# Kernel tuning notes

Hardware: AMD Instinct MI355X
Metric: run time of the kernel (lower is better)

The kernel has to match this reference:

```python
import jax, jax.numpy as jnp
import numpy as np

NUM_LEVELS = 8
CODEBOOK_SIZE = 1024
D_MODEL = 512


def setup_inputs() -> dict:
    key = jax.random.key(0)
    kx, kc = jax.random.split(key)
    x = jax.random.normal(kx, (8, 4096, D_MODEL), dtype=jnp.float32)
    # stacked embedding tables, one per RVQ level: [L, K, D]
    codebooks = jax.random.normal(kc, (NUM_LEVELS, CODEBOOK_SIZE, D_MODEL), dtype=jnp.float32)
    return {"x": x, "codebooks": codebooks}


def reference(x, codebooks):
    """Residual VQ: per level, nearest-codebook lookup on the residual.

    x: [B, N, D], codebooks: [L, K, D].
    Returns (quantized [B, N, D] with straight-through estimator, indices [B, N, L]).
    """
    residual = x
    q_sum = jnp.zeros_like(x)
    all_indices = []
    for l in range(codebooks.shape[0]):
        cb = codebooks[l]  # [K, D]
        # squared Euclidean distance; argmin matches torch.cdist argmin
        r2 = jnp.sum(residual * residual, axis=-1, keepdims=True)      # [B, N, 1]
        c2 = jnp.sum(cb * cb, axis=-1)                                  # [K]
        cross = jnp.einsum("bnd,kd->bnk", residual, cb)                # [B, N, K]
        dist2 = r2 - 2.0 * cross + c2                                   # [B, N, K]
        idx = jnp.argmin(dist2, axis=-1)                                # [B, N]
        all_indices.append(idx)
        q = cb[idx]                                                     # gather: [B, N, D]
        q_sum = q_sum + q
        residual = residual - q
    # straight-through: forward value is q_sum, gradient flows to x only
    quantized = x + jax.lax.stop_gradient(q_sum - x)
    return quantized, jnp.stack(all_indices, axis=-1)
```

## Files before the change

kernel.cpp:

```cpp
#include <hip/hip_runtime.h>
#include <stdint.h>

#define NLV 8
#define KCB 1024
#define DM  512
#define NTOK (8*4096)
#define BETA 0.00390625f

typedef _Float16 f16;
typedef f16  f16x4 __attribute__((ext_vector_type(4)));
typedef f16  f16x8 __attribute__((ext_vector_type(8)));
typedef float f32x4 __attribute__((ext_vector_type(4)));

typedef __attribute__((address_space(1))) const unsigned int* as1p;
typedef __attribute__((address_space(3))) unsigned int*       as3p;
__device__ __forceinline__ void gll16(const void* g, void* l) {
    __builtin_amdgcn_global_load_lds((as1p)g, (as3p)l, 16, 0, 0);
}

__global__ void c2_kernel(const float* __restrict__ cbs, float* __restrict__ c2) {
    int row  = blockIdx.x;
    int lane = threadIdx.x;
    const float4* p4 = (const float4*)(cbs + (size_t)row * DM);
    float4 a = p4[lane];
    float4 b = p4[lane + 64];
    float s = a.x*a.x + a.y*a.y + a.z*a.z + a.w*a.w
            + b.x*b.x + b.y*b.y + b.z*b.z + b.w*b.w;
    float t = (float)(f16)a.x + (float)(f16)a.y + (float)(f16)a.z + (float)(f16)a.w
            + (float)(f16)b.x + (float)(f16)b.y + (float)(f16)b.z + (float)(f16)b.w;
    #pragma unroll
    for (int off = 32; off > 0; off >>= 1) {
        s += __shfl_down(s, off, 64);
        t += __shfl_down(t, off, 64);
    }
    if (lane == 0) c2[row] = s + 2.0f * BETA * t;
}

__global__ void split_kernel(const float* __restrict__ src,
                             f16* __restrict__ hi, f16* __restrict__ lo) {
    size_t i = (size_t)blockIdx.x * 256 + threadIdx.x;
    float4 v = ((const float4*)src)[i];
    f16x4 h, l;
    h.x = (f16)v.x; l.x = (f16)((v.x - (float)h.x) + BETA);
    h.y = (f16)v.y; l.y = (f16)((v.y - (float)h.y) + BETA);
    h.z = (f16)v.z; l.z = (f16)((v.z - (float)h.z) + BETA);
    h.w = (f16)v.w; l.w = (f16)((v.w - (float)h.w) + BETA);
    ((f16x4*)hi)[i] = h;
    ((f16x4*)lo)[i] = l;
}

#define MBT  128
#define NCH  256
#define KS   32
#define NTHR 512
#define BUFB 49152

__global__ __launch_bounds__(NTHR, 2)
void rvq_mfma(const float* __restrict__ xin, float* __restrict__ qout,
              const float* __restrict__ cbs,
              const f16* __restrict__ Bhi, const f16* __restrict__ Blo,
              f16* __restrict__ Ahi, f16* __restrict__ Alo,
              const float* __restrict__ c2g, float* __restrict__ idxout,
              int lvl, int is_last)
{
    __shared__ char smem[2 * BUFB];
    const int tid  = threadIdx.x;
    const int lane = tid & 63;
    const int w    = tid >> 6;
    const int wn   = w & 3;
    const int wm   = w >> 2;
    const int tx   = lane & 15;
    const int q    = lane >> 4;
    const size_t tok0 = (size_t)blockIdx.x * MBT;

    const f16*   Bh_l = Bhi + (size_t)lvl * KCB * DM;
    const f16*   Bl_l = Blo + (size_t)lvl * KCB * DM;
    const float* c2l  = c2g + lvl * KCB;
    const float* cbl  = cbs + (size_t)lvl * KCB * DM;

    const int rloc = lane >> 2;
    const int sg   = (lane & 3) ^ ((lane >> 3) & 3);
    const int rsw  = q ^ ((tx >> 1) & 3);

    const f16* pAh = Ahi + (tok0 + w * 16 + rloc) * (size_t)DM + sg * 8;
    const f16* pAl = Alo + (tok0 + w * 16 + rloc) * (size_t)DM + sg * 8;
    const size_t bRow = (size_t)(w * 16 + rloc) * DM + sg * 8;

    auto stage = [&](char* buf, int gk2) {
        const int ko    = (gk2 & 15) * KS;
        const size_t bo = (size_t)((gk2 >> 4) * NCH) * DM + ko;
        gll16(pAh + ko, buf + w * 1024);
        gll16(pAl + ko, buf + 8192 + w * 1024);
        gll16(Bh_l + bo + bRow,            buf + 16384 + w * 1024);
        gll16(Bh_l + bo + bRow + 128 * DM, buf + 16384 + (w + 8) * 1024);
        gll16(Bl_l + bo + bRow,            buf + 32768 + w * 1024);
        gll16(Bl_l + bo + bRow + 128 * DM, buf + 32768 + (w + 8) * 1024);
    };

    int aoff[4], boff[4];
    #pragma unroll
    for (int i = 0; i < 4; ++i) aoff[i] = (wm * 64 + i * 16 + tx) * 64 + rsw * 16;
    #pragma unroll
    for (int j = 0; j < 4; ++j) boff[j] = (wn * 64 + j * 16 + tx) * 64 + rsw * 16;

    float bestv[16];
    int   besti[16];
    #pragma unroll
    for (int t = 0; t < 16; ++t) { bestv[t] = 3.4e38f; besti[t] = 0; }

    stage(smem, 0);

    for (int ch = 0; ch < KCB / NCH; ++ch) {
        f32x4 acc[4][4];
        #pragma unroll
        for (int i = 0; i < 4; ++i)
            #pragma unroll
            for (int j = 0; j < 4; ++j) acc[i][j] = (f32x4)0.0f;

        for (int kk = 0; kk < 16; ++kk) {
            const int gk = ch * 16 + kk;
            char* bb = smem + (gk & 1) * BUFB;
            char* bn = smem + ((gk & 1) ^ 1) * BUFB;

            __syncthreads();
            if (gk + 1 < 64)
                stage(bn, gk + 1);

            f16x8 ah[4], al[4], bh[4], bl[4];
            #pragma unroll
            for (int i = 0; i < 4; ++i) {
                ah[i] = *(const f16x8*)(bb + aoff[i]);
                al[i] = *(const f16x8*)(bb + 8192 + aoff[i]);
            }
            #pragma unroll
            for (int j = 0; j < 4; ++j) {
                bh[j] = *(const f16x8*)(bb + 16384 + boff[j]);
                bl[j] = *(const f16x8*)(bb + 32768 + boff[j]);
            }

            __builtin_amdgcn_s_setprio(1);
            #pragma unroll
            for (int j = 0; j < 4; ++j)
                #pragma unroll
                for (int i = 0; i < 4; ++i)
                    acc[i][j] = __builtin_amdgcn_mfma_f32_16x16x32_f16(ah[i], bh[j], acc[i][j], 0, 0, 0);
            #pragma unroll
            for (int j = 0; j < 4; ++j)
                #pragma unroll
                for (int i = 0; i < 4; ++i)
                    acc[i][j] = __builtin_amdgcn_mfma_f32_16x16x32_f16(ah[i], bl[j], acc[i][j], 0, 0, 0);
            #pragma unroll
            for (int j = 0; j < 4; ++j)
                #pragma unroll
                for (int i = 0; i < 4; ++i)
                    acc[i][j] = __builtin_amdgcn_mfma_f32_16x16x32_f16(al[i], bh[j], acc[i][j], 0, 0, 0);
            __builtin_amdgcn_s_setprio(0);
        }

        const int cb0 = ch * NCH;
        #pragma unroll
        for (int j = 0; j < 4; ++j) {
            int n = cb0 + wn * 64 + j * 16 + tx;
            float c2v = c2l[n];
            #pragma unroll
            for (int i = 0; i < 4; ++i)
                #pragma unroll
                for (int r = 0; r < 4; ++r) {
                    float s = fmaf(-2.f, acc[i][j][r], c2v);
                    int t = i * 4 + r;
                    if (s < bestv[t]) { bestv[t] = s; besti[t] = n; }
                }
        }
    }

    #pragma unroll
    for (int t = 0; t < 16; ++t) {
        float v = bestv[t]; int bi = besti[t];
        #pragma unroll
        for (int off = 1; off < 16; off <<= 1) {
            float ov = __shfl_xor(v, off, 64);
            int   oi = __shfl_xor(bi, off, 64);
            if (ov < v || (ov == v && oi < bi)) { v = ov; bi = oi; }
        }
        bestv[t] = v; besti[t] = bi;
    }

    float* redV = (float*)smem;
    int*   redI = (int*)(smem + 2048);
    int*   kbst = (int*)(smem + 4096);
    __syncthreads();
    if (tx == 0) {
        #pragma unroll
        for (int i = 0; i < 4; ++i)
            #pragma unroll
            for (int r = 0; r < 4; ++r) {
                int m = wm * 64 + i * 16 + q * 4 + r;
                redV[wn * 128 + m] = bestv[i * 4 + r];
                redI[wn * 128 + m] = besti[i * 4 + r];
            }
    }
    __syncthreads();
    if (tid < MBT) {
        float bv = redV[tid]; int bi = redI[tid];
        #pragma unroll
        for (int ww = 1; ww < 4; ++ww) {
            float v  = redV[ww * 128 + tid];
            int   ii = redI[ww * 128 + tid];
            if (v < bv || (v == bv && ii < bi)) { bv = v; bi = ii; }
        }
        kbst[tid] = bi;
        idxout[(tok0 + tid) * NLV + lvl] = (float)bi;
    }
    __syncthreads();

    #pragma unroll 4
    for (int it = 0; it < 16; ++it) {
        int e  = it * NTHR + tid;
        int t  = e >> 6, d8 = e & 63;
        size_t go = (tok0 + t) * (size_t)DM + d8 * 8;
        f16x8 h8 = *(const f16x8*)&Ahi[go];
        f16x8 l8 = *(const f16x8*)&Alo[go];
        const float* cp = &cbl[(size_t)kbst[t] * DM + d8 * 8];
        float4 c0 = *(const float4*)cp;
        float4 c1 = *(const float4*)(cp + 4);
        float r[8];
        r[0] = (float)h8[0] + ((float)l8[0] - BETA) - c0.x;
        r[1] = (float)h8[1] + ((float)l8[1] - BETA) - c0.y;
        r[2] = (float)h8[2] + ((float)l8[2] - BETA) - c0.z;
        r[3] = (float)h8[3] + ((float)l8[3] - BETA) - c0.w;
        r[4] = (float)h8[4] + ((float)l8[4] - BETA) - c1.x;
        r[5] = (float)h8[5] + ((float)l8[5] - BETA) - c1.y;
        r[6] = (float)h8[6] + ((float)l8[6] - BETA) - c1.z;
        r[7] = (float)h8[7] + ((float)l8[7] - BETA) - c1.w;
        if (is_last) {
            float4 x0 = *(const float4*)&xin[go];
            float4 x1 = *(const float4*)&xin[go + 4];
            float4 q0 = make_float4(x0.x - r[0], x0.y - r[1], x0.z - r[2], x0.w - r[3]);
            float4 q1 = make_float4(x1.x - r[4], x1.y - r[5], x1.z - r[6], x1.w - r[7]);
            *(float4*)&qout[go]     = q0;
            *(float4*)&qout[go + 4] = q1;
        } else {
            f16x8 h, l;
            #pragma unroll
            for (int k = 0; k < 8; ++k) {
                h[k] = (f16)r[k];
                l[k] = (f16)((r[k] - (float)h[k]) + BETA);
            }
            *(f16x8*)&Ahi[go] = h;
            *(f16x8*)&Alo[go] = l;
        }
    }
}

extern "C" void kernel_launch(void* const* d_in, const int* in_sizes, int n_in,
                              void* d_out, int out_size, void* d_ws, size_t ws_size,
                              hipStream_t stream) {
    const float* x   = (const float*)d_in[0];
    const float* cbs = (const float*)d_in[1];
    float* qout   = (float*)d_out;
    float* idxout = qout + (size_t)NTOK * DM;

    const size_t B_ELE = (size_t)NLV * KCB * DM;
    const size_t A_ELE = (size_t)NTOK * DM;

    f16* Bhi = (f16*)d_ws;
    f16* Blo = Bhi + B_ELE;
    f16* Ahi = Blo + B_ELE;
    f16* Alo = Ahi + A_ELE;
    float* c2 = (float*)(Alo + A_ELE);

    split_kernel<<<(int)(B_ELE / 4 / 256), 256, 0, stream>>>(cbs, Bhi, Blo);
    split_kernel<<<(int)(A_ELE / 4 / 256), 256, 0, stream>>>(x, Ahi, Alo);
    c2_kernel<<<NLV * KCB, 64, 0, stream>>>(cbs, c2);

    const int nblocks = NTOK / MBT;
    for (int l = 0; l < NLV; ++l) {
        rvq_mfma<<<nblocks, NTHR, 0, stream>>>(x, qout, cbs,
                                               Bhi, Blo, Ahi, Alo, c2, idxout,
                                               l, (l == NLV - 1) ? 1 : 0);
    }
}
```

Measured before the change: 1.128 ms.

## Triple-buffer LDS staging and prefetch next step's hi fragments into registers

Moves LDS staging from a double to a triple buffer so global-to-LDS loads run two k-steps ahead. The hi-part A/B fragments for the next step are read into registers during the current step, with even/odd register sets swapped through an unrolled pair of loop bodies. The aim is to hide LDS read latency and load stalls behind the MFMA chain. In exchange, LDS per block grows to 147 KB, which may fail to fit two blocks per CU as launch_bounds requests, and register pressure rises.

After: 1.117 ms. No clear change (-1.0%).

```diff
diff --git a/kernel.cpp b/kernel.cpp
--- a/kernel.cpp
+++ b/kernel.cpp
@@ -63,7 +63,7 @@
               const float* __restrict__ c2g, float* __restrict__ idxout,
               int lvl, int is_last)
 {
-    __shared__ char smem[2 * BUFB];
+    __shared__ char smem[3 * BUFB];
     const int tid  = threadIdx.x;
     const int lane = tid & 63;
     const int w    = tid >> 6;
@@ -108,7 +108,58 @@
     #pragma unroll
     for (int t = 0; t < 16; ++t) { bestv[t] = 3.4e38f; besti[t] = 0; }
 
+    f16x8 ahE[4], bhE[4], ahO[4], bhO[4];
+
     stage(smem, 0);
+    __syncthreads();
+    stage(smem + BUFB, 1);
+    #pragma unroll
+    for (int i = 0; i < 4; ++i) ahE[i] = *(const f16x8*)(smem + aoff[i]);
+    #pragma unroll
+    for (int j = 0; j < 4; ++j) bhE[j] = *(const f16x8*)(smem + 16384 + boff[j]);
+
+    auto kbody = [&](int gk, f32x4 (&acc)[4][4],
+                     f16x8 (&ahC)[4], f16x8 (&bhC)[4],
+                     f16x8 (&ahN)[4], f16x8 (&bhN)[4]) {
+        char* bufC = smem + (gk % 3) * BUFB;
+        char* bufR = smem + ((gk + 1) % 3) * BUFB;
+        char* bufS = smem + ((gk + 2) % 3) * BUFB;
+
+        __syncthreads();
+        if (gk + 2 < 64) stage(bufS, gk + 2);
+
+        f16x8 al[4], bl[4];
+        #pragma unroll
+        for (int i = 0; i < 4; ++i) al[i] = *(const f16x8*)(bufC + 8192 + aoff[i]);
+        #pragma unroll
+        for (int j = 0; j < 4; ++j) bl[j] = *(const f16x8*)(bufC + 32768 + boff[j]);
+
+        if (gk + 1 < 64) {
+            #pragma unroll
+            for (int i = 0; i < 4; ++i) ahN[i] = *(const f16x8*)(bufR + aoff[i]);
+            #pragma unroll
+            for (int j = 0; j < 4; ++j) bhN[j] = *(const f16x8*)(bufR + 16384 + boff[j]);
+        }
+        __builtin_amdgcn_sched_barrier(0);
+
+        __builtin_amdgcn_s_setprio(1);
+        #pragma unroll
+        for (int j = 0; j < 4; ++j)
+            #pragma unroll
+            for (int i = 0; i < 4; ++i)
+                acc[i][j] = __builtin_amdgcn_mfma_f32_16x16x32_f16(ahC[i], bhC[j], acc[i][j], 0, 0, 0);
+        #pragma unroll
+        for (int j = 0; j < 4; ++j)
+            #pragma unroll
+            for (int i = 0; i < 4; ++i)
+                acc[i][j] = __builtin_amdgcn_mfma_f32_16x16x32_f16(ahC[i], bl[j], acc[i][j], 0, 0, 0);
+        #pragma unroll
+        for (int j = 0; j < 4; ++j)
+            #pragma unroll
+            for (int i = 0; i < 4; ++i)
+                acc[i][j] = __builtin_amdgcn_mfma_f32_16x16x32_f16(al[i], bhC[j], acc[i][j], 0, 0, 0);
+        __builtin_amdgcn_s_setprio(0);
+    };
 
     for (int ch = 0; ch < KCB / NCH; ++ch) {
         f32x4 acc[4][4];
@@ -117,44 +168,10 @@
             #pragma unroll
             for (int j = 0; j < 4; ++j) acc[i][j] = (f32x4)0.0f;
 
-        for (int kk = 0; kk < 16; ++kk) {
-            const int gk = ch * 16 + kk;
-            char* bb = smem + (gk & 1) * BUFB;
-            char* bn = smem + ((gk & 1) ^ 1) * BUFB;
-
-            __syncthreads();
-            if (gk + 1 < 64)
-                stage(bn, gk + 1);
-
-            f16x8 ah[4], al[4], bh[4], bl[4];
-            #pragma unroll
-            for (int i = 0; i < 4; ++i) {
-                ah[i] = *(const f16x8*)(bb + aoff[i]);
-                al[i] = *(const f16x8*)(bb + 8192 + aoff[i]);
-            }
-            #pragma unroll
-            for (int j = 0; j < 4; ++j) {
-                bh[j] = *(const f16x8*)(bb + 16384 + boff[j]);
-                bl[j] = *(const f16x8*)(bb + 32768 + boff[j]);
-            }
-
-            __builtin_amdgcn_s_setprio(1);
-            #pragma unroll
-            for (int j = 0; j < 4; ++j)
-                #pragma unroll
-                for (int i = 0; i < 4; ++i)
-                    acc[i][j] = __builtin_amdgcn_mfma_f32_16x16x32_f16(ah[i], bh[j], acc[i][j], 0, 0, 0);
-            #pragma unroll
-            for (int j = 0; j < 4; ++j)
-                #pragma unroll
-                for (int i = 0; i < 4; ++i)
-                    acc[i][j] = __builtin_amdgcn_mfma_f32_16x16x32_f16(ah[i], bl[j], acc[i][j], 0, 0, 0);
-            #pragma unroll
-            for (int j = 0; j < 4; ++j)
-                #pragma unroll
-                for (int i = 0; i < 4; ++i)
-                    acc[i][j] = __builtin_amdgcn_mfma_f32_16x16x32_f16(al[i], bh[j], acc[i][j], 0, 0, 0);
-            __builtin_amdgcn_s_setprio(0);
+        for (int kp = 0; kp < 8; ++kp) {
+            const int gk = ch * 16 + kp * 2;
+            kbody(gk,     acc, ahE, bhE, ahO, bhO);
+            kbody(gk + 1, acc, ahO, bhO, ahE, bhE);
         }
 
         const int cb0 = ch * NCH;
```

## Fuse all RVQ levels into one persistent kernel with cross-level prefetch

Applied to the files above, without the earlier changes.

The eight per-level launches are folded into a single kernel that loops over levels inside each block. Each block owns its 128 tokens, so no grid-wide sync is needed. The first codebook tile of the next level is prefetched during the argmin reduction, and the A tile is restaged after a threadfence. The aim is to remove launch gaps and the pipeline drain and refill between levels. In exchange the block-local residual writes must be made visible through global memory with a fence before they are reloaded.

After: 1.361 ms. 20.6% more time.

```diff
diff --git a/kernel.cpp b/kernel.cpp
--- a/kernel.cpp
+++ b/kernel.cpp
@@ -56,12 +56,11 @@
 #define BUFB 49152
 
 __global__ __launch_bounds__(NTHR, 2)
-void rvq_mfma(const float* __restrict__ xin, float* __restrict__ qout,
-              const float* __restrict__ cbs,
-              const f16* __restrict__ Bhi, const f16* __restrict__ Blo,
-              f16* __restrict__ Ahi, f16* __restrict__ Alo,
-              const float* __restrict__ c2g, float* __restrict__ idxout,
-              int lvl, int is_last)
+void rvq_fused(const float* __restrict__ xin, float* __restrict__ qout,
+               const float* __restrict__ cbs,
+               const f16* __restrict__ Bhi, const f16* __restrict__ Blo,
+               f16* __restrict__ Ahi, f16* __restrict__ Alo,
+               const float* __restrict__ c2g, float* __restrict__ idxout)
 {
     __shared__ char smem[2 * BUFB];
     const int tid  = threadIdx.x;
@@ -73,11 +72,6 @@
     const int q    = lane >> 4;
     const size_t tok0 = (size_t)blockIdx.x * MBT;
 
-    const f16*   Bh_l = Bhi + (size_t)lvl * KCB * DM;
-    const f16*   Bl_l = Blo + (size_t)lvl * KCB * DM;
-    const float* c2l  = c2g + lvl * KCB;
-    const float* cbl  = cbs + (size_t)lvl * KCB * DM;
-
     const int rloc = lane >> 2;
     const int sg   = (lane & 3) ^ ((lane >> 3) & 3);
     const int rsw  = q ^ ((tx >> 1) & 3);
@@ -85,17 +79,6 @@
     const f16* pAh = Ahi + (tok0 + w * 16 + rloc) * (size_t)DM + sg * 8;
     const f16* pAl = Alo + (tok0 + w * 16 + rloc) * (size_t)DM + sg * 8;
     const size_t bRow = (size_t)(w * 16 + rloc) * DM + sg * 8;
-
-    auto stage = [&](char* buf, int gk2) {
-        const int ko    = (gk2 & 15) * KS;
-        const size_t bo = (size_t)((gk2 >> 4) * NCH) * DM + ko;
-        gll16(pAh + ko, buf + w * 1024);
-        gll16(pAl + ko, buf + 8192 + w * 1024);
-        gll16(Bh_l + bo + bRow,            buf + 16384 + w * 1024);
-        gll16(Bh_l + bo + bRow + 128 * DM, buf + 16384 + (w + 8) * 1024);
-        gll16(Bl_l + bo + bRow,            buf + 32768 + w * 1024);
-        gll16(Bl_l + bo + bRow + 128 * DM, buf + 32768 + (w + 8) * 1024);
-    };
 
     int aoff[4], boff[4];
     #pragma unroll
@@ -103,151 +86,187 @@
     #pragma unroll
     for (int j = 0; j < 4; ++j) boff[j] = (wn * 64 + j * 16 + tx) * 64 + rsw * 16;
 
-    float bestv[16];
-    int   besti[16];
-    #pragma unroll
-    for (int t = 0; t < 16; ++t) { bestv[t] = 3.4e38f; besti[t] = 0; }
-
-    stage(smem, 0);
-
-    for (int ch = 0; ch < KCB / NCH; ++ch) {
-        f32x4 acc[4][4];
+    float* redV = (float*)(smem + BUFB);
+    int*   redI = (int*)(smem + BUFB + 2048);
+    int*   kbst = (int*)(smem + BUFB + 4096);
+
+    for (int lvl = 0; lvl < NLV; ++lvl) {
+        const f16*   Bh_l = Bhi + (size_t)lvl * KCB * DM;
+        const f16*   Bl_l = Blo + (size_t)lvl * KCB * DM;
+        const float* c2l  = c2g + lvl * KCB;
+        const float* cbl  = cbs + (size_t)lvl * KCB * DM;
+
+        auto stageB = [&](char* buf, int gk2, const f16* bh_p, const f16* bl_p) {
+            const int ko    = (gk2 & 15) * KS;
+            const size_t bo = (size_t)((gk2 >> 4) * NCH) * DM + ko;
+            gll16(bh_p + bo + bRow,            buf + 16384 + w * 1024);
+            gll16(bh_p + bo + bRow + 128 * DM, buf + 16384 + (w + 8) * 1024);
+            gll16(bl_p + bo + bRow,            buf + 32768 + w * 1024);
+            gll16(bl_p + bo + bRow + 128 * DM, buf + 32768 + (w + 8) * 1024);
+        };
+        auto stageA = [&](char* buf, int gk2) {
+            const int ko = (gk2 & 15) * KS;
+            gll16(pAh + ko, buf + w * 1024);
+            gll16(pAl + ko, buf + 8192 + w * 1024);
+        };
+
+        if (lvl == 0) {
+            stageB(smem, 0, Bh_l, Bl_l);
+            stageA(smem, 0);
+        }
+
+        float bestv[16];
+        int   besti[16];
         #pragma unroll
-        for (int i = 0; i < 4; ++i)
-            #pragma unroll
-            for (int j = 0; j < 4; ++j) acc[i][j] = (f32x4)0.0f;
-
-        for (int kk = 0; kk < 16; ++kk) {
-            const int gk = ch * 16 + kk;
-            char* bb = smem + (gk & 1) * BUFB;
-            char* bn = smem + ((gk & 1) ^ 1) * BUFB;
-
+        for (int t = 0; t < 16; ++t) { bestv[t] = 3.4e38f; besti[t] = 0; }
+
+        for (int ch = 0; ch < KCB / NCH; ++ch) {
+            f32x4 acc[4][4];
+            #pragma unroll
+            for (int i = 0; i < 4; ++i)
+                #pragma unroll
+                for (int j = 0; j < 4; ++j) acc[i][j] = (f32x4)0.0f;
+
+            for (int kk = 0; kk < 16; ++kk) {
+                const int gk = ch * 16 + kk;
+                char* bb = smem + (gk & 1) * BUFB;
+                char* bn = smem + ((gk & 1) ^ 1) * BUFB;
+
+                __syncthreads();
+                if (gk + 1 < 64) {
+                    stageB(bn, gk + 1, Bh_l, Bl_l);
+                    stageA(bn, gk + 1);
+                }
+
+                f16x8 ah[4], al[4], bh[4], bl[4];
+                #pragma unroll
+                for (int i = 0; i < 4; ++i) {
+                    ah[i] = *(const f16x8*)(bb + aoff[i]);
+                    al[i] = *(const f16x8*)(bb + 8192 + aoff[i]);
+                }
+                #pragma unroll
+                for (int j = 0; j < 4; ++j) {
+                    bh[j] = *(const f16x8*)(bb + 16384 + boff[j]);
+                    bl[j] = *(const f16x8*)(bb + 32768 + boff[j]);
+                }
+
+                __builtin_amdgcn_s_setprio(1);
+                #pragma unroll
+                for (int j = 0; j < 4; ++j)
+                    #pragma unroll
+                    for (int i = 0; i < 4; ++i)
+                        acc[i][j] = __builtin_amdgcn_mfma_f32_16x16x32_f16(ah[i], bh[j], acc[i][j], 0, 0, 0);
+                #pragma unroll
+                for (int j = 0; j < 4; ++j)
+                    #pragma unroll
+                    for (int i = 0; i < 4; ++i)
+                        acc[i][j] = __builtin_amdgcn_mfma_f32_16x16x32_f16(ah[i], bl[j], acc[i][j], 0, 0, 0);
+                #pragma unroll
+                for (int j = 0; j < 4; ++j)
+                    #pragma unroll
+                    for (int i = 0; i < 4; ++i)
+                        acc[i][j] = __builtin_amdgcn_mfma_f32_16x16x32_f16(al[i], bh[j], acc[i][j], 0, 0, 0);
+                __builtin_amdgcn_s_setprio(0);
+            }
+
+            const int cb0 = ch * NCH;
+            #pragma unroll
+            for (int j = 0; j < 4; ++j) {
+                int n = cb0 + wn * 64 + j * 16 + tx;
+                float c2v = c2l[n];
+                #pragma unroll
+                for (int i = 0; i < 4; ++i)
+                    #pragma unroll
+                    for (int r = 0; r < 4; ++r) {
+                        float s = fmaf(-2.f, acc[i][j][r], c2v);
+                        int t = i * 4 + r;
+                        if (s < bestv[t]) { bestv[t] = s; besti[t] = n; }
+                    }
+            }
+        }
+
+        #pragma unroll
+        for (int t = 0; t < 16; ++t) {
+            float v = bestv[t]; int bi = besti[t];
+            #pragma unroll
+            for (int off = 1; off < 16; off <<= 1) {
+                float ov = __shfl_xor(v, off, 64);
+                int   oi = __shfl_xor(bi, off, 64);
+                if (ov < v || (ov == v && oi < bi)) { v = ov; bi = oi; }
+            }
+            bestv[t] = v; besti[t] = bi;
+        }
+
+        __syncthreads();
+        if (lvl + 1 < NLV)
+            stageB(smem, 0, Bh_l + (size_t)KCB * DM, Bl_l + (size_t)KCB * DM);
+        if (tx == 0) {
+            #pragma unroll
+            for (int i = 0; i < 4; ++i)
+                #pragma unroll
+                for (int r = 0; r < 4; ++r) {
+                    int m = wm * 64 + i * 16 + q * 4 + r;
+                    redV[wn * 128 + m] = bestv[i * 4 + r];
+                    redI[wn * 128 + m] = besti[i * 4 + r];
+                }
+        }
+        __syncthreads();
+        if (tid < MBT) {
+            float bv = redV[tid]; int bi = redI[tid];
+            #pragma unroll
+            for (int ww = 1; ww < 4; ++ww) {
+                float v  = redV[ww * 128 + tid];
+                int   ii = redI[ww * 128 + tid];
+                if (v < bv || (v == bv && ii < bi)) { bv = v; bi = ii; }
+            }
+            kbst[tid] = bi;
+            idxout[(tok0 + tid) * NLV + lvl] = (float)bi;
+        }
+        __syncthreads();
+
+        const int is_last = (lvl == NLV - 1);
+        #pragma unroll 4
+        for (int it = 0; it < 16; ++it) {
+            int e  = it * NTHR + tid;
+            int t  = e >> 6, d8 = e & 63;
+            size_t go = (tok0 + t) * (size_t)DM + d8 * 8;
+            f16x8 h8 = *(const f16x8*)&Ahi[go];
+            f16x8 l8 = *(const f16x8*)&Alo[go];
+            const float* cp = &cbl[(size_t)kbst[t] * DM + d8 * 8];
+            float4 c0 = *(const float4*)cp;
+            float4 c1 = *(const float4*)(cp + 4);
+            float r[8];
+            r[0] = (float)h8[0] + ((float)l8[0] - BETA) - c0.x;
+            r[1] = (float)h8[1] + ((float)l8[1] - BETA) - c0.y;
+            r[2] = (float)h8[2] + ((float)l8[2] - BETA) - c0.z;
+            r[3] = (float)h8[3] + ((float)l8[3] - BETA) - c0.w;
+            r[4] = (float)h8[4] + ((float)l8[4] - BETA) - c1.x;
+            r[5] = (float)h8[5] + ((float)l8[5] - BETA) - c1.y;
+            r[6] = (float)h8[6] + ((float)l8[6] - BETA) - c1.z;
+            r[7] = (float)h8[7] + ((float)l8[7] - BETA) - c1.w;
+            if (is_last) {
+                float4 x0 = *(const float4*)&xin[go];
+                float4 x1 = *(const float4*)&xin[go + 4];
+                float4 q0 = make_float4(x0.x - r[0], x0.y - r[1], x0.z - r[2], x0.w - r[3]);
+                float4 q1 = make_float4(x1.x - r[4], x1.y - r[5], x1.z - r[6], x1.w - r[7]);
+                *(float4*)&qout[go]     = q0;
+                *(float4*)&qout[go + 4] = q1;
+            } else {
+                f16x8 h, l;
+                #pragma unroll
+                for (int k = 0; k < 8; ++k) {
+                    h[k] = (f16)r[k];
+                    l[k] = (f16)((r[k] - (float)h[k]) + BETA);
+                }
+                *(f16x8*)&Ahi[go] = h;
+                *(f16x8*)&Alo[go] = l;
+            }
+        }
+
+        if (lvl + 1 < NLV) {
+            __threadfence();
             __syncthreads();
-            if (gk + 1 < 64)
-                stage(bn, gk + 1);
-
-            f16x8 ah[4], al[4], bh[4], bl[4];
-            #pragma unroll
-            for (int i = 0; i < 4; ++i) {
-                ah[i] = *(const f16x8*)(bb + aoff[i]);
-                al[i] = *(const f16x8*)(bb + 8192 + aoff[i]);
-            }
-            #pragma unroll
-            for (int j = 0; j < 4; ++j) {
-                bh[j] = *(const f16x8*)(bb + 16384 + boff[j]);
-                bl[j] = *(const f16x8*)(bb + 32768 + boff[j]);
-            }
-
-            __builtin_amdgcn_s_setprio(1);
-            #pragma unroll
-            for (int j = 0; j < 4; ++j)
-                #pragma unroll
-                for (int i = 0; i < 4; ++i)
-                    acc[i][j] = __builtin_amdgcn_mfma_f32_16x16x32_f16(ah[i], bh[j], acc[i][j], 0, 0, 0);
-            #pragma unroll
-            for (int j = 0; j < 4; ++j)
-                #pragma unroll
-                for (int i = 0; i < 4; ++i)
-                    acc[i][j] = __builtin_amdgcn_mfma_f32_16x16x32_f16(ah[i], bl[j], acc[i][j], 0, 0, 0);
-            #pragma unroll
-            for (int j = 0; j < 4; ++j)
-                #pragma unroll
-                for (int i = 0; i < 4; ++i)
-                    acc[i][j] = __builtin_amdgcn_mfma_f32_16x16x32_f16(al[i], bh[j], acc[i][j], 0, 0, 0);
-            __builtin_amdgcn_s_setprio(0);
-        }
-
-        const int cb0 = ch * NCH;
-        #pragma unroll
-        for (int j = 0; j < 4; ++j) {
-            int n = cb0 + wn * 64 + j * 16 + tx;
-            float c2v = c2l[n];
-            #pragma unroll
-            for (int i = 0; i < 4; ++i)
-                #pragma unroll
-                for (int r = 0; r < 4; ++r) {
-                    float s = fmaf(-2.f, acc[i][j][r], c2v);
-                    int t = i * 4 + r;
-                    if (s < bestv[t]) { bestv[t] = s; besti[t] = n; }
-                }
-        }
-    }
-
-    #pragma unroll
-    for (int t = 0; t < 16; ++t) {
-        float v = bestv[t]; int bi = besti[t];
-        #pragma unroll
-        for (int off = 1; off < 16; off <<= 1) {
-            float ov = __shfl_xor(v, off, 64);
-            int   oi = __shfl_xor(bi, off, 64);
-            if (ov < v || (ov == v && oi < bi)) { v = ov; bi = oi; }
-        }
-        bestv[t] = v; besti[t] = bi;
-    }
-
-    float* redV = (float*)smem;
-    int*   redI = (int*)(smem + 2048);
-    int*   kbst = (int*)(smem + 4096);
-    __syncthreads();
-    if (tx == 0) {
-        #pragma unroll
-        for (int i = 0; i < 4; ++i)
-            #pragma unroll
-            for (int r = 0; r < 4; ++r) {
-                int m = wm * 64 + i * 16 + q * 4 + r;
-                redV[wn * 128 + m] = bestv[i * 4 + r];
-                redI[wn * 128 + m] = besti[i * 4 + r];
-            }
-    }
-    __syncthreads();
-    if (tid < MBT) {
-        float bv = redV[tid]; int bi = redI[tid];
-        #pragma unroll
-        for (int ww = 1; ww < 4; ++ww) {
-            float v  = redV[ww * 128 + tid];
-            int   ii = redI[ww * 128 + tid];
-            if (v < bv || (v == bv && ii < bi)) { bv = v; bi = ii; }
-        }
-        kbst[tid] = bi;
-        idxout[(tok0 + tid) * NLV + lvl] = (float)bi;
-    }
-    __syncthreads();
-
-    #pragma unroll 4
-    for (int it = 0; it < 16; ++it) {
-        int e  = it * NTHR + tid;
-        int t  = e >> 6, d8 = e & 63;
-        size_t go = (tok0 + t) * (size_t)DM + d8 * 8;
-        f16x8 h8 = *(const f16x8*)&Ahi[go];
-        f16x8 l8 = *(const f16x8*)&Alo[go];
-        const float* cp = &cbl[(size_t)kbst[t] * DM + d8 * 8];
-        float4 c0 = *(const float4*)cp;
-        float4 c1 = *(const float4*)(cp + 4);
-        float r[8];
-        r[0] = (float)h8[0] + ((float)l8[0] - BETA) - c0.x;
-        r[1] = (float)h8[1] + ((float)l8[1] - BETA) - c0.y;
-        r[2] = (float)h8[2] + ((float)l8[2] - BETA) - c0.z;
-        r[3] = (float)h8[3] + ((float)l8[3] - BETA) - c0.w;
-        r[4] = (float)h8[4] + ((float)l8[4] - BETA) - c1.x;
-        r[5] = (float)h8[5] + ((float)l8[5] - BETA) - c1.y;
-        r[6] = (float)h8[6] + ((float)l8[6] - BETA) - c1.z;
-        r[7] = (float)h8[7] + ((float)l8[7] - BETA) - c1.w;
-        if (is_last) {
-            float4 x0 = *(const float4*)&xin[go];
-            float4 x1 = *(const float4*)&xin[go + 4];
-            float4 q0 = make_float4(x0.x - r[0], x0.y - r[1], x0.z - r[2], x0.w - r[3]);
-            float4 q1 = make_float4(x1.x - r[4], x1.y - r[5], x1.z - r[6], x1.w - r[7]);
-            *(float4*)&qout[go]     = q0;
-            *(float4*)&qout[go + 4] = q1;
-        } else {
-            f16x8 h, l;
-            #pragma unroll
-            for (int k = 0; k < 8; ++k) {
-                h[k] = (f16)r[k];
-                l[k] = (f16)((r[k] - (float)h[k]) + BETA);
-            }
-            *(f16x8*)&Ahi[go] = h;
-            *(f16x8*)&Alo[go] = l;
+            stageA(smem, 0);
         }
     }
 }
@@ -273,10 +292,6 @@
     split_kernel<<<(int)(A_ELE / 4 / 256), 256, 0, stream>>>(x, Ahi, Alo);
     c2_kernel<<<NLV * KCB, 64, 0, stream>>>(cbs, c2);
 
-    const int nblocks = NTOK / MBT;
-    for (int l = 0; l < NLV; ++l) {
-        rvq_mfma<<<nblocks, NTHR, 0, stream>>>(x, qout, cbs,
-                                               Bhi, Blo, Ahi, Alo, c2, idxout,
-                                               l, (l == NLV - 1) ? 1 : 0);
-    }
-}
+    rvq_fused<<<NTOK / MBT, NTHR, 0, stream>>>(x, qout, cbs,
+                                               Bhi, Blo, Ahi, Alo, c2, idxout);
+}
```
